# Performance work log

Measured on AMD Instinct MI355X. Metric: run time of the kernel, lower is better.

Reference implementation:

```python
import jax, jax.numpy as jnp
import numpy as np

B, S, D, H, FF = 4, 1024, 1024, 8, 4096
DK = D // H
EPS = 1e-5


def layernorm(x, g, b):
    m = jnp.mean(x, axis=-1, keepdims=True)
    v = jnp.mean(jnp.square(x - m), axis=-1, keepdims=True)
    return (x - m) * jax.lax.rsqrt(v + EPS) * g + b


def setup_inputs() -> dict:
    key = jax.random.key(0)
    ks = jax.random.split(key, 8)
    w = lambda k, shape: jax.random.normal(k, shape, jnp.float32) * 0.02
    return {
        "x": jax.random.normal(ks[0], (B, S, D), jnp.float32),
        "mask": jnp.ones((B, 1, 1, S), jnp.int32),  # unused in 'infer' mode, kept for fidelity
        "g1": jnp.ones((D,), jnp.float32), "b1": jnp.zeros((D,), jnp.float32),
        "Wq": w(ks[1], (D, D)), "bq": jnp.zeros((D,), jnp.float32),
        "Wk": w(ks[2], (D, D)), "bk": jnp.zeros((D,), jnp.float32),
        "Wv": w(ks[3], (D, H * D)), "bv": jnp.zeros((H * D,), jnp.float32),
        "g2": jnp.ones((D,), jnp.float32), "b2": jnp.zeros((D,), jnp.float32),
        "W1": w(ks[4], (D, FF)), "bw1": jnp.zeros((FF,), jnp.float32),
        "W2": w(ks[5], (FF, D)), "bw2": jnp.zeros((D,), jnp.float32),
    }


def reference(x, mask, g1, b1, Wq, bq, Wk, bk, Wv, bv, g2, b2, W1, bw1, W2, bw2):
    # --- MultiHeadedAttention (mode='infer'; mask is ignored by this path) ---
    xn = layernorm(x, g1, b1)                                   # [B,S,D]
    q = (xn @ Wq + bq).reshape(B, S, H, DK).transpose(0, 2, 1, 3)  # [B,H,S,DK]
    k = (xn @ Wk + bk).reshape(B, S, H, DK).transpose(0, 2, 1, 3)  # [B,H,S,DK]
    v = (xn @ Wv + bv).reshape(B, S, H, D).transpose(0, 2, 1, 3)   # [B,H,S,D]
    scores = jnp.einsum('bhqd,bhkd->bhqk', q, k) / jnp.sqrt(jnp.float32(DK))
    p = jax.nn.softmax(scores, axis=-1)                          # [B,H,S,S]
    ctx = jnp.einsum('bhqk,bhkd->bhqd', p, v)                    # [B,H,S,D]
    # Source does x.view(-1, B, dim, h).sum(heads).view(B, S, dim) on the
    # contiguous [B,H,S,D] tensor: a raw row-major reshape, reproduced exactly.
    attn_out = ctx.reshape(S, B, D, H).sum(axis=-1).reshape(B, S, D)
    # --- residual + SublayerConnection (pre-norm GELU FFN) ---
    x1 = x + attn_out
    xn2 = layernorm(x1, g2, b2)
    ffn = jax.nn.gelu(xn2 @ W1 + bw1, approximate=False) @ W2 + bw2
    return x1 + ffn
```

## Files before the change

### kernel.cpp

```cpp
#include <hip/hip_runtime.h>
#include <hip/hip_bf16.h>
#include <math.h>

typedef __attribute__((ext_vector_type(8))) short   short8;
typedef __attribute__((ext_vector_type(4))) short   short4v;
typedef __attribute__((ext_vector_type(8))) __bf16  bf16x8;
typedef __attribute__((ext_vector_type(4))) float   f32x4;

typedef const __attribute__((address_space(1))) void cgv_t;
typedef __attribute__((address_space(3))) void lv_t;

__device__ __forceinline__ float bs2f(short s) {
  unsigned int u = ((unsigned int)(unsigned short)s) << 16;
  return __builtin_bit_cast(float, u);
}
__device__ __forceinline__ short f2bs(float f) {
  __hip_bfloat16 h = __float2bfloat16(f);
  return __builtin_bit_cast(short, h);
}
__device__ __forceinline__ void glds16(const short* g, short* l) {
  __builtin_amdgcn_global_load_lds((cgv_t*)g, (lv_t*)l, 16, 0, 0);
}


struct TrU { const float* in; short* out; int R, C, bx, by; };

__device__ __forceinline__ TrU tr_decode(
    int u,
    const float* Wq, short* wqT, const float* Wk, short* wkT,
    const float* W1, short* w1T, const float* W2, short* w2T) {
  TrU s;
  if (u < 1024)      { s.in = W1; s.out = w1T; s.R = 1024; s.C = 4096; s.bx = u & 63; s.by = u >> 6; }
  else if (u < 2048) { int v = u - 1024; s.in = W2; s.out = w2T; s.R = 4096; s.C = 1024; s.bx = v & 15; s.by = v >> 4; }
  else if (u < 2304) { int v = u - 2048; s.in = Wq; s.out = wqT; s.R = 1024; s.C = 1024; s.bx = v & 15; s.by = v >> 4; }
  else               { int v = u - 2304; s.in = Wk; s.out = wkT; s.R = 1024; s.C = 1024; s.bx = v & 15; s.by = v >> 4; }
  return s;
}

__device__ __forceinline__ void tr2_body(const TrU& A, const TrU& B,
                                         short* T0, short* T1) {
  const int t = threadIdx.x;
  const int rr = t >> 4, cc = (t & 15) << 2;
  f32x4 va[4], vb[4];
#pragma unroll
  for (int h = 0; h < 4; h++)
    va[h] = *(const f32x4*)(A.in + (long)(A.by * 64 + rr + h * 16) * A.C + A.bx * 64 + cc);
#pragma unroll
  for (int h = 0; h < 4; h++)
    vb[h] = *(const f32x4*)(B.in + (long)(B.by * 64 + rr + h * 16) * B.C + B.bx * 64 + cc);
#pragma unroll
  for (int h = 0; h < 4; h++)
#pragma unroll
    for (int e = 0; e < 4; e++) {
      T0[(rr + h * 16) * 72 + cc + e] = f2bs(va[h][e]);
      T1[(rr + h * 16) * 72 + cc + e] = f2bs(vb[h][e]);
    }
  __syncthreads();
  const int cr = t >> 3, rs = (t & 7) << 3;
#pragma unroll
  for (int hf = 0; hf < 2; hf++) {
    const int c = cr + hf * 32;
    short8 v0, v1;
#pragma unroll
    for (int e = 0; e < 8; e++) { v0[e] = T0[(rs + e) * 72 + c]; v1[e] = T1[(rs + e) * 72 + c]; }
    *(short8*)(A.out + (long)(A.bx * 64 + c) * A.R + A.by * 64 + rs) = v0;
    *(short8*)(B.out + (long)(B.bx * 64 + c) * B.R + B.by * 64 + rs) = v1;
  }
}

__device__ __forceinline__ void wv8_body(const float* __restrict__ Wv,
                                         short* __restrict__ out,
                                         int bx, int by, short* T) {
  const int r0 = bx * 64, k0 = by * 64;
  const int t = threadIdx.x;
  const int wave = t >> 6, lane = t & 63;
  const int r = r0 + lane;
#pragma unroll 4
  for (int i = 0; i < 16; i++) {
    const int k = k0 + wave * 16 + i;
    const float* src = Wv + (long)k * 8192 + 8 * r;
    f32x4 a = *(const f32x4*)src;
    f32x4 b = *(const f32x4*)(src + 4);
    float s = (a[0] + a[1] + a[2] + a[3]) + (b[0] + b[1] + b[2] + b[3]);
    T[lane * 72 + wave * 16 + i] = f2bs(s);
  }
  __syncthreads();
  const int rr = t >> 3, kc = (t & 7) << 3;
#pragma unroll
  for (int half = 0; half < 2; half++) {
    const int rl = rr + half * 32;
    *(short8*)(out + (long)(r0 + rl) * 1024 + k0 + kc) = *(const short8*)&T[rl * 72 + kc];
  }
}

__device__ __forceinline__ void ln_body(const float* __restrict__ in,
                                        const float* __restrict__ g,
                                        const float* __restrict__ b,
                                        short* __restrict__ out, int row,
                                        float* rs, float* rq) {
  const int t = threadIdx.x;
  const long base = (long)row * 1024 + t * 4;
  f32x4 f = *(const f32x4*)(in + base);
  float v[4] = {f[0], f[1], f[2], f[3]};
  float s1 = v[0] + v[1] + v[2] + v[3];
  float s2 = v[0]*v[0] + v[1]*v[1] + v[2]*v[2] + v[3]*v[3];
#pragma unroll
  for (int off = 32; off; off >>= 1) {
    s1 += __shfl_xor(s1, off);
    s2 += __shfl_xor(s2, off);
  }
  if ((t & 63) == 0) { rs[t >> 6] = s1; rq[t >> 6] = s2; }
  __syncthreads();
  s1 = rs[0] + rs[1] + rs[2] + rs[3];
  s2 = rq[0] + rq[1] + rq[2] + rq[3];
  const float mean = s1 * (1.0f / 1024.0f);
  const float var  = s2 * (1.0f / 1024.0f) - mean * mean;
  const float rstd = rsqrtf(var + 1e-5f);
  f32x4 gv = *(const f32x4*)(g + t * 4);
  f32x4 bv = *(const f32x4*)(b + t * 4);
  short4v o;
#pragma unroll
  for (int i = 0; i < 4; i++)
    o[i] = f2bs((v[i] - mean) * rstd * gv[i] + bv[i]);
  *(short4v*)(out + base) = o;
}

__global__ __launch_bounds__(256) void prep_k(
    const float* __restrict__ x, const float* __restrict__ g1,
    const float* __restrict__ b1, short* __restrict__ xn,
    const float* __restrict__ Wq, short* __restrict__ wqT,
    const float* __restrict__ Wk, short* __restrict__ wkT,
    const float* __restrict__ Wv, short* __restrict__ wv8T,
    const float* __restrict__ W1, short* __restrict__ w1T,
    const float* __restrict__ W2, short* __restrict__ w2T,
    const float* __restrict__ bq, const float* __restrict__ bk,
    const float* __restrict__ bv, float* __restrict__ bQKV) {
  __shared__ __align__(16) short T[2][64 * 72];
  __shared__ float rs[4], rq[4];
  const int t = threadIdx.x;
  int bid = blockIdx.x;
  if (bid < 1280) {
    TrU A = tr_decode(bid * 2,     Wq, wqT, Wk, wkT, W1, w1T, W2, w2T);
    TrU B = tr_decode(bid * 2 + 1, Wq, wqT, Wk, wkT, W1, w1T, W2, w2T);
    tr2_body(A, B, T[0], T[1]);
    return;
  }
  bid -= 1280;
  if (bid < 256) { wv8_body(Wv, wv8T, bid & 15, bid >> 4, T[0]); return; }
  bid -= 256;
  if (bid < 4) {
    const int r = bid * 256 + t;
    f32x4 a = *(const f32x4*)(bv + 8 * r);
    f32x4 b = *(const f32x4*)(bv + 8 * r + 4);
    bQKV[2048 + r] = (a[0] + a[1] + a[2] + a[3]) + (b[0] + b[1] + b[2] + b[3]);
    return;
  }
  bid -= 4;
  if (bid == 0) { *(f32x4*)(bQKV + t * 4) = *(const f32x4*)(bq + t * 4); return; }
  if (bid == 1) { *(f32x4*)(bQKV + 1024 + t * 4) = *(const f32x4*)(bk + t * 4); return; }
  ln_body(x, g1, b1, xn, bid - 2, rs, rq);
}

__global__ __launch_bounds__(256) void ln_k(const float* __restrict__ in,
                                            const float* __restrict__ g,
                                            const float* __restrict__ b,
                                            short* __restrict__ out) {
  __shared__ float rs[4], rq[4];
  ln_body(in, g, b, out, blockIdx.x, rs, rq);
}

__global__ __launch_bounds__(256) void reduce4_k(const float* __restrict__ p,
                                                 const float* __restrict__ x1,
                                                 const float* __restrict__ bias,
                                                 float* __restrict__ out) {
  const int t = threadIdx.x;
  const long base = (long)blockIdx.x * 1024 + t * 4;
  f32x4 a = *(const f32x4*)(p + base);
  f32x4 b = *(const f32x4*)(p + 4194304 + base);
  f32x4 c = *(const f32x4*)(p + 8388608 + base);
  f32x4 d = *(const f32x4*)(p + 12582912 + base);
  f32x4 e = *(const f32x4*)(x1 + base);
  f32x4 g = *(const f32x4*)(bias + t * 4);
  *(f32x4*)(out + base) = a + b + c + d + e + g;
}

__global__ __launch_bounds__(256, 2) void flash_k(
    const short* __restrict__ Qg_, const short* __restrict__ Kg_,
    const short* __restrict__ V8T, const float* __restrict__ xg,
    float* __restrict__ x1) {
  __shared__ __align__(16) short smem[40960];
  short* Qs = smem;
  short* Ks = smem + 8192;
  short* Vs = smem + 24576;

  const int t = threadIdx.x;
  const int wave = t >> 6, lane = t & 63;
  const int llo = lane & 15, lhi = lane >> 4;

  int lin = blockIdx.x + (blockIdx.y << 4);
  lin = (lin & 7) * 64 + (lin >> 3);
  const int q0 = (lin & 15) * 64;
  const int bh = lin >> 4, b = bh >> 3, h = bh & 7;

  const short* Qg = Qg_ + ((long)(b * 1024 + q0)) * 1024 + h * 128;
  const short* Kg = Kg_ + ((long)b * 1024) * 1024 + h * 128;
  const short* Vg = V8T + (long)bh * 131072;

  const int srow = t >> 2;
  const int sgc = (((t & 3) ^ ((t >> 3) & 3)) << 3);
  const int wbase = wave * 512;
  const int swzo = ((lhi ^ ((llo >> 1) & 3)) << 3);
  const int arow = (wave * 16 + llo) * 32 + swzo;

#pragma unroll
  for (int kk = 0; kk < 4; kk++)
    glds16(Qg + (long)srow * 1024 + kk * 32 + sgc, Qs + kk * 2048 + wbase);

  f32x4 o[8];
  float mR[4], lR[4];
#pragma unroll
  for (int i = 0; i < 8; i++) o[i] = f32x4{0.f, 0.f, 0.f, 0.f};
#pragma unroll
  for (int r = 0; r < 4; r++) { mR[r] = -1e30f; lR[r] = 0.f; }

  for (int it = 0; it < 8; it++) {
    const int kt0 = it * 128;
#pragma unroll
    for (int kk = 0; kk < 4; kk++) {
      glds16(Kg + (long)(kt0 + srow) * 1024 + kk * 32 + sgc,
             Ks + kk * 4096 + wbase);
      glds16(Kg + (long)(kt0 + 64 + srow) * 1024 + kk * 32 + sgc,
             Ks + kk * 4096 + 2048 + wbase);
      glds16(Vg + (long)srow * 1024 + kt0 + kk * 32 + sgc,
             Vs + kk * 4096 + wbase);
      glds16(Vg + (long)(64 + srow) * 1024 + kt0 + kk * 32 + sgc,
             Vs + kk * 4096 + 2048 + wbase);
    }
    __syncthreads();

    f32x4 s[8];
#pragma unroll
    for (int i = 0; i < 8; i++) s[i] = f32x4{0.f, 0.f, 0.f, 0.f};
#pragma unroll
    for (int kk = 0; kk < 4; kk++) {
      bf16x8 aq = *(const bf16x8*)(Qs + kk * 2048 + arow);
#pragma unroll
      for (int ct = 0; ct < 8; ct++) {
        bf16x8 bk = *(const bf16x8*)(Ks + kk * 4096 + (ct * 16 + llo) * 32 + swzo);
        s[ct] = __builtin_amdgcn_mfma_f32_16x16x32_bf16(aq, bk, s[ct], 0, 0, 0);
      }
    }
    float mt[4];
#pragma unroll
    for (int r = 0; r < 4; r++) {
      float m = s[0][r];
#pragma unroll
      for (int ct = 1; ct < 8; ct++) m = fmaxf(m, s[ct][r]);
      m = fmaxf(m, __shfl_xor(m, 1));
      m = fmaxf(m, __shfl_xor(m, 2));
      m = fmaxf(m, __shfl_xor(m, 4));
      m = fmaxf(m, __shfl_xor(m, 8));
      mt[r] = m;
    }
    bool need = (mt[0] > mR[0] + 8.f) | (mt[1] > mR[1] + 8.f) |
                (mt[2] > mR[2] + 8.f) | (mt[3] > mR[3] + 8.f);
    if (__any(need)) {
      float alpha[4];
#pragma unroll
      for (int r = 0; r < 4; r++) {
        const float mn = fmaxf(mR[r], mt[r]);
        alpha[r] = __builtin_amdgcn_exp2f(mR[r] - mn);
        mR[r] = mn;
        lR[r] *= alpha[r];
      }
#pragma unroll
      for (int ct = 0; ct < 8; ct++)
#pragma unroll
        for (int r = 0; r < 4; r++) o[ct][r] *= alpha[r];
    }
#pragma unroll
    for (int ct = 0; ct < 8; ct++)
#pragma unroll
      for (int r = 0; r < 4; r++)
        s[ct][r] = __builtin_amdgcn_exp2f(s[ct][r] - mR[r]);
#pragma unroll
    for (int r = 0; r < 4; r++) {
      float ls = s[0][r];
#pragma unroll
      for (int ct = 1; ct < 8; ct++) ls += s[ct][r];
      ls += __shfl_xor(ls, 1);
      ls += __shfl_xor(ls, 2);
      ls += __shfl_xor(ls, 4);
      ls += __shfl_xor(ls, 8);
      lR[r] += ls;
    }
    __syncthreads();

#pragma unroll
    for (int ct = 0; ct < 8; ct++) {
      const int chunk = ((ct & 1) << 1) | (llo >> 3);
      const int cl = llo & 7;
#pragma unroll
      for (int r = 0; r < 4; r++) {
        const int row = wave * 16 + lhi * 4 + r;
        const int xr = ((lhi << 1) | (r >> 1)) & 3;
        Ks[(ct >> 1) * 4096 + row * 32 + (((chunk ^ xr) << 3) | cl)] = f2bs(s[ct][r]);
      }
    }
    __syncthreads();

#pragma unroll
    for (int kk = 0; kk < 4; kk++) {
      bf16x8 ap = *(const bf16x8*)(Ks + kk * 4096 + arow);
#pragma unroll
      for (int ct = 0; ct < 8; ct++) {
        bf16x8 bv = *(const bf16x8*)(Vs + kk * 4096 + (ct * 16 + llo) * 32 + swzo);
        o[ct] = __builtin_amdgcn_mfma_f32_16x16x32_bf16(ap, bv, o[ct], 0, 0, 0);
      }
    }
    __syncthreads();
  }

  float inv[4];
#pragma unroll
  for (int r = 0; r < 4; r++) inv[r] = 1.0f / lR[r];
#pragma unroll
  for (int ct = 0; ct < 8; ct++) {
#pragma unroll
    for (int r = 0; r < 4; r++) {
      const int row = q0 + wave * 16 + lhi * 4 + r;
      const long idx = ((long)(b * 8 + h) * 1024 + row) * 128 + ct * 16 + llo;
      x1[idx] = xg[idx] + o[ct][r] * inv[r];
    }
  }
}

enum { E_GELU = 0, E_QKV = 1, E_PART = 2 };

#define MF16(va, vb, vc) __builtin_amdgcn_mfma_f32_16x16x32_bf16(va, vb, vc, 0, 0, 0)
#define VMW(n) asm volatile("s_waitcnt vmcnt(" #n ")" ::: "memory")
#define NOPS ((void)0)

#define STAGE_A(BUF, KH, KB) do {                                          \
    glds16(Ag + (KB), smem + ((BUF) * 2 + (KH)) * 8192 + wofs);            \
    glds16(Ag2 + (KB), smem + ((BUF) * 2 + (KH)) * 8192 + 4096 + wofs);    \
  } while (0)
#define STAGE_B(BUF, KH, KB) do {                                          \
    glds16(Bg + (KB), smem + 32768 + ((BUF) * 2 + (KH)) * 8192 + wofs);    \
    glds16(Bg2 + (KB), smem + 32768 + ((BUF) * 2 + (KH)) * 8192 + 4096 + wofs); \
  } while (0)

#define PHASE(RH, KH, BUF, LOADB, STAGE_STMT, WAIT_STMT)                   \
  {                                                                        \
    const short* Ar_ = smem + ((BUF) * 2 + (KH)) * 8192 + aoff + (RH) * 2048; \
    bf16x8 a0 = *(const bf16x8*)(Ar_);                                     \
    bf16x8 a1 = *(const bf16x8*)(Ar_ + 512);                               \
    bf16x8 a2 = *(const bf16x8*)(Ar_ + 1024);                              \
    bf16x8 a3 = *(const bf16x8*)(Ar_ + 1536);                              \
    if (LOADB) {                                                           \
      const short* Br_ = smem + 32768 + ((BUF) * 2 + (KH)) * 8192 + boff;  \
      vb0 = *(const bf16x8*)(Br_);                                         \
      vb1 = *(const bf16x8*)(Br_ + 512);                                   \
      vb2 = *(const bf16x8*)(Br_ + 1024);                                  \
      vb3 = *(const bf16x8*)(Br_ + 1536);                                  \
    }                                                                      \
    STAGE_STMT;                                                            \
    __builtin_amdgcn_s_setprio(1);                                         \
    acc[(RH) * 4 + 0][0] = MF16(a0, vb0, acc[(RH) * 4 + 0][0]);            \
    acc[(RH) * 4 + 0][1] = MF16(a0, vb1, acc[(RH) * 4 + 0][1]);            \
    acc[(RH) * 4 + 0][2] = MF16(a0, vb2, acc[(RH) * 4 + 0][2]);            \
    acc[(RH) * 4 + 0][3] = MF16(a0, vb3, acc[(RH) * 4 + 0][3]);            \
    acc[(RH) * 4 + 1][0] = MF16(a1, vb0, acc[(RH) * 4 + 1][0]);            \
    acc[(RH) * 4 + 1][1] = MF16(a1, vb1, acc[(RH) * 4 + 1][1]);            \
    acc[(RH) * 4 + 1][2] = MF16(a1, vb2, acc[(RH) * 4 + 1][2]);            \
    acc[(RH) * 4 + 1][3] = MF16(a1, vb3, acc[(RH) * 4 + 1][3]);            \
    acc[(RH) * 4 + 2][0] = MF16(a2, vb0, acc[(RH) * 4 + 2][0]);            \
    acc[(RH) * 4 + 2][1] = MF16(a2, vb1, acc[(RH) * 4 + 2][1]);            \
    acc[(RH) * 4 + 2][2] = MF16(a2, vb2, acc[(RH) * 4 + 2][2]);            \
    acc[(RH) * 4 + 2][3] = MF16(a2, vb3, acc[(RH) * 4 + 2][3]);            \
    acc[(RH) * 4 + 3][0] = MF16(a3, vb0, acc[(RH) * 4 + 3][0]);            \
    acc[(RH) * 4 + 3][1] = MF16(a3, vb1, acc[(RH) * 4 + 3][1]);            \
    acc[(RH) * 4 + 3][2] = MF16(a3, vb2, acc[(RH) * 4 + 3][2]);            \
    acc[(RH) * 4 + 3][3] = MF16(a3, vb3, acc[(RH) * 4 + 3][3]);            \
    __builtin_amdgcn_s_setprio(0);                                         \
    WAIT_STMT;                                                             \
    __builtin_amdgcn_sched_barrier(0);                                     \
    __builtin_amdgcn_s_barrier();                                          \
    __builtin_amdgcn_sched_barrier(0);                                     \
  }

#define TILE8(T, BUF)                                                        \
  PHASE(0, 0, BUF, 1, STAGE_A(1 - (BUF), 1, ((T) + 1) * 64 + 32), NOPS);     \
  PHASE(1, 0, BUF, 0, STAGE_B(1 - (BUF), 1, ((T) + 1) * 64 + 32), VMW(8));   \
  PHASE(0, 1, BUF, 1, STAGE_A(BUF, 0, ((T) + 2) * 64), NOPS);                \
  PHASE(1, 1, BUF, 0, STAGE_B(BUF, 0, ((T) + 2) * 64), VMW(8))

template <int EPI>
__global__ __launch_bounds__(512, 2) void gemm256(
    const short* __restrict__ A, int lda, long azk,
    const short* __restrict__ Bt, int ldb, long bzk,
    const float* __restrict__ bias, long biasl,
    void* __restrict__ outp, long czl, int ldc,
    void* __restrict__ aux, int K) {
  __shared__ __align__(16) short smem[65536];

  const int t = threadIdx.x;
  const int wave = t >> 6, lane = t & 63;
  const int llo = lane & 15, lhi = lane >> 4;
  const int wm = wave >> 2, wn = wave & 3;

  int lin = blockIdx.x + gridDim.x * (blockIdx.y + gridDim.y * blockIdx.z);
  const int nwg = gridDim.x * gridDim.y * gridDim.z;
  lin = (lin & 7) * (nwg >> 3) + (lin >> 3);
  const int bx = lin % gridDim.x;
  const int rem = lin / gridDim.x;
  const int by = rem % gridDim.y;
  const int z = rem / gridDim.y;

  const int bm0 = by * 256, bn0 = bx * 256;
  A += (long)z * azk;
  Bt += (long)z * bzk;

  const int srow = t >> 2;
  const int sgc = (((t & 3) ^ ((t >> 3) & 3)) << 3);
  const short* Ag  = A  + (long)(bm0 + srow) * lda + sgc;
  const short* Ag2 = A  + (long)(bm0 + 128 + srow) * lda + sgc;
  const short* Bg  = Bt + (long)(bn0 + srow) * ldb + sgc;
  const short* Bg2 = Bt + (long)(bn0 + 128 + srow) * ldb + sgc;
  const int wofs = wave * 512;

  const int swz = ((lhi ^ ((llo >> 1) & 3)) << 3);
  const int aoff = (wm * 128 + llo) * 32 + swz;
  const int boff = (wn * 64 + llo) * 32 + swz;

  f32x4 acc[8][4];
#pragma unroll
  for (int i = 0; i < 8; i++)
#pragma unroll
    for (int j = 0; j < 4; j++) acc[i][j] = f32x4{0.f, 0.f, 0.f, 0.f};
  bf16x8 vb0, vb1, vb2, vb3;

  const int NT = K >> 6;

  STAGE_A(0, 0, 0);  STAGE_B(0, 0, 0);
  STAGE_A(0, 1, 32); STAGE_B(0, 1, 32);
  STAGE_A(1, 0, 64); STAGE_B(1, 0, 64);
  VMW(8);
  __builtin_amdgcn_sched_barrier(0);
  __builtin_amdgcn_s_barrier();
  __builtin_amdgcn_sched_barrier(0);

  for (int tt = 0; tt < NT - 2; tt += 2) {
    TILE8(tt, 0);
    TILE8(tt + 1, 1);
  }
  PHASE(0, 0, 0, 1, STAGE_A(1, 1, (NT - 1) * 64 + 32), NOPS);
  PHASE(1, 0, 0, 0, STAGE_B(1, 1, (NT - 1) * 64 + 32), VMW(8));
  PHASE(0, 1, 0, 1, NOPS, NOPS);
  PHASE(1, 1, 0, 0, NOPS, VMW(4));
  PHASE(0, 0, 1, 1, NOPS, NOPS);
  PHASE(1, 0, 1, 0, NOPS, VMW(0));
  PHASE(0, 1, 1, 1, NOPS, NOPS);
  PHASE(1, 1, 1, 0, NOPS, NOPS);

  if (EPI == E_PART) {
    float* P = (float*)outp + (long)z * czl;
#pragma unroll
    for (int ct = 0; ct < 4; ct++) {
      const int col = bn0 + wn * 64 + ct * 16 + llo;
#pragma unroll
      for (int rt = 0; rt < 8; rt++) {
#pragma unroll
        for (int r = 0; r < 4; r++) {
          const int row = bm0 + wm * 128 + rt * 16 + lhi * 4 + r;
          P[(long)row * ldc + col] = acc[rt][ct][r];
        }
      }
    }
  } else if (EPI == E_QKV && z == 2) {
    short* slab = smem + wave * 4352;
    const int bb = bm0 >> 10, sbase = (bm0 & 1023) + wm * 128;
    float bv4[4];
#pragma unroll
    for (int ct = 0; ct < 4; ct++)
      bv4[ct] = bias[z * biasl + bn0 + wn * 64 + ct * 16 + llo];
    const int gcol = bn0 + wn * 64 + lane;
    short* dst0 = (short*)aux + ((long)(bb * 8 + (gcol >> 7))) * 131072 +
                  (long)(gcol & 127) * 1024 + sbase;
#pragma unroll
    for (int p = 0; p < 2; p++) {
#pragma unroll
      for (int rt4 = 0; rt4 < 4; rt4++) {
#pragma unroll
        for (int ct = 0; ct < 4; ct++) {
#pragma unroll
          for (int r = 0; r < 4; r++) {
            float v = acc[p * 4 + rt4][ct][r] + bv4[ct];
            slab[(ct * 16 + llo) * 68 + rt4 * 16 + lhi * 4 + r] = f2bs(v);
          }
        }
      }
#pragma unroll
      for (int j = 0; j < 8; j++)
        *(short8*)(dst0 + p * 64 + j * 8) = *(const short8*)&slab[lane * 68 + j * 8];
    }
  } else {
    short* C = (short*)outp + (long)z * czl;
    short* slab = smem + wave * 4864;
    float bv4[4];
#pragma unroll
    for (int ct = 0; ct < 4; ct++)
      bv4[ct] = bias[z * biasl + bn0 + wn * 64 + ct * 16 + llo];
    const int rl0 = lane >> 3, cb8 = (lane & 7) << 3;
    const short* srd = slab + rl0 * 76 + cb8;
    short* Cw = C + (long)(bm0 + wm * 128 + rl0) * ldc + bn0 + wn * 64 + cb8;
#pragma unroll
    for (int p = 0; p < 2; p++) {
#pragma unroll
      for (int rt4 = 0; rt4 < 4; rt4++) {
#pragma unroll
        for (int ct = 0; ct < 4; ct++) {
#pragma unroll
          for (int r = 0; r < 4; r++) {
            float v = acc[p * 4 + rt4][ct][r] + bv4[ct];
            if (EPI == E_GELU)
              v = 0.5f * v * (1.0f + erff(v * 0.70710678118654752f));
            if (EPI == E_QKV && z == 0)
              v *= 0.12751744476582f;
            slab[(rt4 * 16 + lhi * 4 + r) * 76 + ct * 16 + llo] = f2bs(v);
          }
        }
      }
#pragma unroll
      for (int j = 0; j < 8; j++) {
        short8 v = *(const short8*)(srd + j * 8 * 76);
        *(short8*)(Cw + ((long)p * 64 + j * 8) * ldc) = v;
      }
    }
  }
}

extern "C" void kernel_launch(void* const* d_in, const int* in_sizes, int n_in,
                              void* d_out, int out_size, void* d_ws, size_t ws_size,
                              hipStream_t stream) {
  const float* x   = (const float*)d_in[0];
  const float* g1  = (const float*)d_in[2];
  const float* b1  = (const float*)d_in[3];
  const float* Wq  = (const float*)d_in[4];
  const float* bq  = (const float*)d_in[5];
  const float* Wk  = (const float*)d_in[6];
  const float* bk  = (const float*)d_in[7];
  const float* Wv  = (const float*)d_in[8];
  const float* bv  = (const float*)d_in[9];
  const float* g2  = (const float*)d_in[10];
  const float* b2  = (const float*)d_in[11];
  const float* W1  = (const float*)d_in[12];
  const float* bw1 = (const float*)d_in[13];
  const float* W2  = (const float*)d_in[14];
  const float* bw2 = (const float*)d_in[15];

  char* ws = (char*)d_ws;
  const long MB = 1024 * 1024;
  float* bQKV  = (float*)(ws);
  float* x1    = (float*)(ws + 1 * MB);
  short* wqT   = (short*)(ws + 17 * MB);
  short* wkT   = (short*)(ws + 19 * MB);
  short* wv8T  = (short*)(ws + 21 * MB);
  short* xn    = (short*)(ws + 23 * MB);
  short* Q     = (short*)(ws + 31 * MB);
  short* Kb    = (short*)(ws + 39 * MB);
  short* V8T   = (short*)(ws + 47 * MB);
  short* xn2  = (short*)(ws + 17 * MB);
  short* Hb   = (short*)(ws + 25 * MB);
  short* w1T  = (short*)(ws + 57 * MB);
  short* w2T  = (short*)(ws + 65 * MB);
  float* part = (float*)(ws + 73 * MB);

  prep_k<<<5638, 256, 0, stream>>>(x, g1, b1, xn,
                                   Wq, wqT, Wk, wkT, Wv, wv8T,
                                   W1, w1T, W2, w2T,
                                   bq, bk, bv, bQKV);

  gemm256<E_QKV><<<dim3(4, 16, 3), 512, 0, stream>>>(
      xn, 1024, 0, wqT, 1024, 1048576, bQKV, 1024,
      Q, 4194304, 1024, V8T, 1024);

  flash_k<<<dim3(16, 32), 256, 0, stream>>>(Q, Kb, V8T, x, x1);

  ln_k<<<4096, 256, 0, stream>>>(x1, g2, b2, xn2);

  gemm256<E_GELU><<<dim3(16, 16, 1), 512, 0, stream>>>(
      xn2, 1024, 0, w1T, 1024, 0, bw1, 0,
      Hb, 0, 4096, nullptr, 1024);

  gemm256<E_PART><<<dim3(4, 16, 4), 512, 0, stream>>>(
      Hb, 4096, 1024, w2T, 4096, 1024, nullptr, 0,
      part, 4194304, 1024, nullptr, 1024);

  reduce4_k<<<4096, 256, 0, stream>>>(part, x1, bw2, (float*)d_out);
}
```

Measured before the change: 348.1 us.

## Add dedicated 128x256-tile GELU GEMM kernel for FFN up-projection

```diff
diff --git a/kernel.cpp b/kernel.cpp
--- a/kernel.cpp
+++ b/kernel.cpp
@@ -523,8 +523,6 @@
 #pragma unroll
           for (int r = 0; r < 4; r++) {
             float v = acc[p * 4 + rt4][ct][r] + bv4[ct];
-            if (EPI == E_GELU)
-              v = 0.5f * v * (1.0f + erff(v * 0.70710678118654752f));
             if (EPI == E_QKV && z == 0)
               v *= 0.12751744476582f;
             slab[(rt4 * 16 + lhi * 4 + r) * 76 + ct * 16 + llo] = f2bs(v);
@@ -538,6 +536,122 @@
       }
     }
   }
+}
+
+__global__ __launch_bounds__(512, 4) void gemm128n_gelu(
+    const short* __restrict__ A, int lda,
+    const short* __restrict__ Bt, int ldb,
+    const float* __restrict__ bias,
+    short* __restrict__ C, int ldc, int K) {
+  __shared__ __align__(16) short smem[38912];
+
+  const int t = threadIdx.x;
+  const int wave = t >> 6, lane = t & 63;
+  const int llo = lane & 15, lhi = lane >> 4;
+  const int wm = wave >> 2, wn = wave & 3;
+
+  int lin = blockIdx.x + (blockIdx.y << 4);
+  lin = (lin & 7) * 64 + (lin >> 3);
+  const int bn0 = (lin & 15) * 256;
+  const int bm0 = (lin >> 4) * 128;
+
+  const int srow = t >> 2;
+  const int sgc = (((t & 3) ^ ((t >> 3) & 3)) << 3);
+  const short* Ag  = A  + (long)(bm0 + srow) * lda + sgc;
+  const short* Bg  = Bt + (long)(bn0 + srow) * ldb + sgc;
+  const short* Bg2 = Bt + (long)(bn0 + 128 + srow) * ldb + sgc;
+  const int wofs = wave * 512;
+
+  const int swz = ((lhi ^ ((llo >> 1) & 3)) << 3);
+  const int aoff = (wm * 64 + llo) * 32 + swz;
+  const int boff = (wn * 64 + llo) * 32 + swz;
+
+  f32x4 acc[4][4];
+#pragma unroll
+  for (int i = 0; i < 4; i++)
+#pragma unroll
+    for (int j = 0; j < 4; j++) acc[i][j] = f32x4{0.f, 0.f, 0.f, 0.f};
+
+#define STG(BUF, KB) do {                                                  \
+    glds16(Ag + (KB), smem + (BUF) * 12288 + wofs);                        \
+    glds16(Bg + (KB), smem + (BUF) * 12288 + 4096 + wofs);                 \
+    glds16(Bg2 + (KB), smem + (BUF) * 12288 + 8192 + wofs);                \
+  } while (0)
+
+#define BODY(BUF, STAGE_STMT, WAIT_STMT)                                   \
+  {                                                                        \
+    const short* Ab_ = smem + (BUF) * 12288 + aoff;                        \
+    const short* Bb_ = smem + (BUF) * 12288 + 4096 + boff;                 \
+    bf16x8 a0 = *(const bf16x8*)(Ab_);                                     \
+    bf16x8 a1 = *(const bf16x8*)(Ab_ + 512);                               \
+    bf16x8 a2 = *(const bf16x8*)(Ab_ + 1024);                              \
+    bf16x8 a3 = *(const bf16x8*)(Ab_ + 1536);                              \
+    bf16x8 b0 = *(const bf16x8*)(Bb_);                                     \
+    bf16x8 b1 = *(const bf16x8*)(Bb_ + 512);                               \
+    bf16x8 b2 = *(const bf16x8*)(Bb_ + 1024);                              \
+    bf16x8 b3 = *(const bf16x8*)(Bb_ + 1536);                              \
+    __builtin_amdgcn_s_setprio(1);                                         \
+    acc[0][0] = MF16(a0, b0, acc[0][0]); acc[0][1] = MF16(a0, b1, acc[0][1]); \
+    acc[0][2] = MF16(a0, b2, acc[0][2]); acc[0][3] = MF16(a0, b3, acc[0][3]); \
+    acc[1][0] = MF16(a1, b0, acc[1][0]); acc[1][1] = MF16(a1, b1, acc[1][1]); \
+    acc[1][2] = MF16(a1, b2, acc[1][2]); acc[1][3] = MF16(a1, b3, acc[1][3]); \
+    acc[2][0] = MF16(a2, b0, acc[2][0]); acc[2][1] = MF16(a2, b1, acc[2][1]); \
+    acc[2][2] = MF16(a2, b2, acc[2][2]); acc[2][3] = MF16(a2, b3, acc[2][3]); \
+    acc[3][0] = MF16(a3, b0, acc[3][0]); acc[3][1] = MF16(a3, b1, acc[3][1]); \
+    acc[3][2] = MF16(a3, b2, acc[3][2]); acc[3][3] = MF16(a3, b3, acc[3][3]); \
+    __builtin_amdgcn_s_setprio(0);                                         \
+    __builtin_amdgcn_sched_barrier(0);                                     \
+    __builtin_amdgcn_s_barrier();                                          \
+    __builtin_amdgcn_sched_barrier(0);                                     \
+    STAGE_STMT;                                                            \
+    WAIT_STMT;                                                             \
+    __builtin_amdgcn_sched_barrier(0);                                     \
+    __builtin_amdgcn_s_barrier();                                          \
+    __builtin_amdgcn_sched_barrier(0);                                     \
+  }
+
+  const int NT = K >> 5;
+
+  STG(0, 0);
+  STG(1, 32);
+  VMW(3);
+  __builtin_amdgcn_sched_barrier(0);
+  __builtin_amdgcn_s_barrier();
+  __builtin_amdgcn_sched_barrier(0);
+
+  for (int i = 0; i < NT - 2; i += 2) {
+    BODY(0, STG(0, (i + 2) * 32), VMW(3));
+    BODY(1, STG(1, (i + 3) * 32), VMW(3));
+  }
+  BODY(0, NOPS, VMW(0));
+  BODY(1, NOPS, NOPS);
+
+  short* slab = smem + wave * 4864;
+  float bv4[4];
+#pragma unroll
+  for (int ct = 0; ct < 4; ct++) bv4[ct] = bias[bn0 + wn * 64 + ct * 16 + llo];
+#pragma unroll
+  for (int rt = 0; rt < 4; rt++) {
+#pragma unroll
+    for (int ct = 0; ct < 4; ct++) {
+#pragma unroll
+      for (int r = 0; r < 4; r++) {
+        float v = acc[rt][ct][r] + bv4[ct];
+        v = 0.5f * v * (1.0f + erff(v * 0.70710678118654752f));
+        slab[(rt * 16 + lhi * 4 + r) * 76 + ct * 16 + llo] = f2bs(v);
+      }
+    }
+  }
+  const int rl0 = lane >> 3, cb8 = (lane & 7) << 3;
+  const short* srd = slab + rl0 * 76 + cb8;
+  short* Cw = C + (long)(bm0 + wm * 64 + rl0) * ldc + bn0 + wn * 64 + cb8;
+#pragma unroll
+  for (int j = 0; j < 8; j++) {
+    short8 v = *(const short8*)(srd + j * 8 * 76);
+    *(short8*)(Cw + (long)(j * 8) * ldc) = v;
+  }
+#undef STG
+#undef BODY
 }
 
 extern "C" void kernel_launch(void* const* d_in, const int* in_sizes, int n_in,
@@ -589,9 +703,8 @@
 
   ln_k<<<4096, 256, 0, stream>>>(x1, g2, b2, xn2);
 
-  gemm256<E_GELU><<<dim3(16, 16, 1), 512, 0, stream>>>(
-      xn2, 1024, 0, w1T, 1024, 0, bw1, 0,
-      Hb, 0, 4096, nullptr, 1024);
+  gemm128n_gelu<<<dim3(16, 32), 512, 0, stream>>>(
+      xn2, 1024, w1T, 1024, bw1, Hb, 4096, 1024);
 
   gemm256<E_PART><<<dim3(4, 16, 4), 512, 0, stream>>>(
       Hb, 4096, 1024, w2T, 4096, 1024, nullptr, 0,
```

Result: faster. 334.7 us (-3.8%).
